# Kernel tuning notes

Hardware: AMD Instinct MI355X
Metric: run time of the kernel (lower is better)

The kernel has to match this reference:

```python
import jax, jax.numpy as jnp
import numpy as np

IN_DIM = 512
OUT_DIM = 256


def setup_inputs() -> dict:
    key = jax.random.key(0)
    ks = jax.random.split(key, 5)
    b, n, d, o = 32, 64, IN_DIM, OUT_DIM
    lim1 = 1.0 / np.sqrt(2 * d)
    lim2 = 1.0 / np.sqrt(o)
    return {
        "x": jax.random.normal(ks[0], (b, n, d), dtype=jnp.float32),
        "W1": jax.random.uniform(ks[1], (o, 2 * d), jnp.float32, -lim1, lim1),
        "b1": jax.random.uniform(ks[2], (o,), jnp.float32, -lim1, lim1),
        "W2": jax.random.uniform(ks[3], (o, o), jnp.float32, -lim2, lim2),
        "b2": jax.random.uniform(ks[4], (o,), jnp.float32, -lim2, lim2),
    }


def reference(x, W1, b1, W2, b2):
    # x: [b, n, d]; fc1 over cat(xi, xj) == xi @ Wa.T + xj @ Wb.T + b1
    b, n, d = x.shape
    Wa, Wb = W1[:, :d], W1[:, d:]
    hi = jnp.einsum("bnd,od->bno", x, Wa)  # [b, n, o]
    hj = jnp.einsum("bnd,od->bno", x, Wb)  # [b, n, o]
    h = hi[:, :, None, :] + hj[:, None, :, :] + b1  # [b, n, n, o]
    y = jax.nn.relu(jnp.einsum("bijo,po->bijp", h, W2) + b2)  # [b, n, n, o]
    mask = ~jnp.eye(n, dtype=bool)  # zero self-pairs
    y = y * mask[None, :, :, None]
    return y.sum(axis=2)  # [b, n, o]
```

## Files before the change

### kernel.cpp

```cpp
#include <hip/hip_runtime.h>
#include <hip/hip_bf16.h>


typedef unsigned short u16;
typedef __attribute__((ext_vector_type(8))) short short8v;
typedef __attribute__((ext_vector_type(4))) short short4v;
typedef __attribute__((ext_vector_type(4))) float float4v;
typedef __attribute__((ext_vector_type(2))) float float2v;

typedef __attribute__((address_space(1))) const unsigned char* gas_ptr;
typedef __attribute__((address_space(3))) unsigned char* las_ptr;

#define FLAG_CONST 0x5EEDF00Du

__device__ __forceinline__ void lds_load16(const void* g, void* l) {
    __builtin_amdgcn_global_load_lds((gas_ptr)g, (las_ptr)l, 16, 0, 0);
}

__device__ __forceinline__ u16 f2bf(float f) {
    unsigned u = __float_as_uint(f);
    return (u16)((u + 0x7fffu + ((u >> 16) & 1u)) >> 16);
}

__device__ __forceinline__ short8v cvt8v(float4v a, float4v b) {
    union { u16 us[8]; short8v v; } o;
    o.us[0] = f2bf(a.x); o.us[1] = f2bf(a.y); o.us[2] = f2bf(a.z); o.us[3] = f2bf(a.w);
    o.us[4] = f2bf(b.x); o.us[5] = f2bf(b.y); o.us[6] = f2bf(b.z); o.us[7] = f2bf(b.w);
    return o.v;
}

#define LDS_TOTAL (66560 + 67584)

__global__ __launch_bounds__(512, 1) void mono_kernel(
    const float* __restrict__ x, const float* __restrict__ W1,
    const float* __restrict__ b1, const float* __restrict__ W2,
    const float* __restrict__ b2,
    u16* __restrict__ Wfb, float* __restrict__ cvec,
    unsigned* __restrict__ flags, float* __restrict__ out) {
    __shared__ __align__(16) unsigned char smem[LDS_TOTAL];
    u16* Xs = (u16*)smem;
    u16* As = (u16*)(smem + 66560);
    u16* Bt = (u16*)(smem + 66560 + 33792);
    u16* Ws = (u16*)(smem + 66560);

    const int bid = blockIdx.x;
    const int tid = threadIdx.x;
    const int lane = tid & 63, w = tid >> 6;
    const int b = ((bid & 7) << 2) | ((bid >> 3) & 3);
    const int pc = bid >> 5;
    const int p0 = pc * 32;
    const int rQ = lane >> 4, rM = lane & 15;

#pragma unroll
    for (int rr = 0; rr < 8; ++rr) {
        int row = w * 8 + rr;
        const float* s = x + (b * 64 + row) * 512 + lane * 8;
        float4v a0 = *(const float4v*)s, a1 = *(const float4v*)(s + 4);
        *(short8v*)&Xs[row * 520 + lane * 8] = cvt8v(a0, a1);
    }

    if (bid < 64) {
        const int q0 = (bid >> 3) * 64;
        const int d0 = (bid & 7) * 64;
        const int pw = q0 & 255;
        const int off = (q0 & 256) * 2;

#pragma unroll
        for (int rr = 0; rr < 4; ++rr) {
            int row = w * 8 + rr * 2 + (lane >> 5);
            int c = lane & 31;
            const float* s = W2 + (pw + row) * 256 + c * 8;
            float4v a0 = *(const float4v*)s, a1 = *(const float4v*)(s + 4);
            *(short8v*)&As[row * 264 + c * 8] = cvt8v(a0, a1);
        }
#pragma unroll
        for (int kk = 0; kk < 2; ++kk) {
            const int m = tid & 15, og = tid >> 4;
            const int o0 = kk * 128 + og * 4;
            const int d4 = m * 4;
            float4v f0 = *(const float4v*)(W1 + (o0 + 0) * 1024 + off + d0 + d4);
            float4v f1 = *(const float4v*)(W1 + (o0 + 1) * 1024 + off + d0 + d4);
            float4v f2 = *(const float4v*)(W1 + (o0 + 2) * 1024 + off + d0 + d4);
            float4v f3 = *(const float4v*)(W1 + (o0 + 3) * 1024 + off + d0 + d4);
            const int u = o0 >> 3, sub = o0 & 7;
#pragma unroll
            for (int dd = 0; dd < 4; ++dd) {
                int d = d4 + dd;
                int usw = u ^ ((d >> 3) & 7);
                union { u16 us[4]; short4v v; } pk;
                pk.us[0] = f2bf(f0[dd]); pk.us[1] = f2bf(f1[dd]);
                pk.us[2] = f2bf(f2[dd]); pk.us[3] = f2bf(f3[dd]);
                *(short4v*)&Bt[d * 264 + usw * 8 + sub] = pk.v;
            }
        }
        __syncthreads();

        const int wm = w >> 1, wn = w & 1;
        float4v pacc[2] = {};
#pragma unroll
        for (int ks = 0; ks < 8; ++ks) {
            short8v a = *(const short8v*)&As[(wm * 16 + rM) * 264 + (ks * 4 + rQ) * 8];
#pragma unroll
            for (int nf = 0; nf < 2; ++nf) {
                int drow = wn * 32 + nf * 16 + rM;
                int ku = (ks * 4 + rQ) ^ ((drow >> 3) & 7);
                short8v bf = *(const short8v*)&Bt[drow * 264 + ku * 8];
                pacc[nf] = __builtin_amdgcn_mfma_f32_16x16x32_bf16(a, bf, pacc[nf], 0, 0, 0);
            }
        }
#pragma unroll
        for (int nf = 0; nf < 2; ++nf)
#pragma unroll
            for (int r = 0; r < 4; ++r) {
                int q = q0 + wm * 16 + rQ * 4 + r;
                int d = d0 + wn * 32 + nf * 16 + rM;
                Wfb[q * 512 + d] = f2bf(pacc[nf][r]);
            }
    } else if (bid == 64 && tid < 256) {
        float acc = b2[tid];
        const float4v* wrow = (const float4v*)(W2 + tid * 256);
#pragma unroll 8
        for (int o4 = 0; o4 < 64; ++o4) {
            float4v wv = wrow[o4];
            float4v bv = *(const float4v*)(b1 + o4 * 4);
            acc += wv.x * bv.x + wv.y * bv.y + wv.z * bv.z + wv.w * bv.w;
        }
        cvec[tid] = acc;
    }

    __syncthreads();
    if (bid <= 64 && tid == 0)
        __hip_atomic_store(&flags[bid * 32], FLAG_CONST, __ATOMIC_RELEASE,
                           __HIP_MEMORY_SCOPE_AGENT);
    if (tid < 65)
        while (__hip_atomic_load(&flags[tid * 32], __ATOMIC_ACQUIRE,
                                 __HIP_MEMORY_SCOPE_AGENT) != FLAG_CONST)
            __builtin_amdgcn_s_sleep(16);
    __syncthreads();

#pragma unroll
    for (int rr = 0; rr < 8; ++rr) {
        int row = w * 8 + rr;
        int q = (row < 32) ? (p0 + row) : (256 + p0 + (row - 32));
        lds_load16(Wfb + q * 512 + lane * 8, (void*)&Ws[row * 520]);
    }
    __syncthreads();

    const int uv = w & 1, rh = w >> 1;
    float4v acc[2] = {};
#pragma unroll
    for (int ks = 0; ks < 16; ++ks) {
        short8v a = *(const short8v*)&Xs[(rh * 16 + rM) * 520 + (ks * 4 + rQ) * 8];
#pragma unroll
        for (int nf = 0; nf < 2; ++nf) {
            int brow = uv * 32 + nf * 16 + rM;
            short8v bf = *(const short8v*)&Ws[brow * 520 + (ks * 4 + rQ) * 8];
            acc[nf] = __builtin_amdgcn_mfma_f32_16x16x32_bf16(a, bf, acc[nf], 0, 0, 0);
        }
    }
    __syncthreads();

    float* Us = (float*)smem;
    float* Vs = Us + 64 * 34;
    float* dst = uv ? Vs : Us;
#pragma unroll
    for (int nf = 0; nf < 2; ++nf)
#pragma unroll
        for (int r = 0; r < 4; ++r)
            dst[(rh * 16 + rQ * 4 + r) * 34 + nf * 16 + rM] = acc[nf][r];
    __syncthreads();

    const int p2 = tid & 15;
    const int ig = tid >> 4;
    float2v cv = *(const float2v*)(cvec + p0 + p2 * 2);
    float2v u2[2], acc2[2];
#pragma unroll
    for (int ii = 0; ii < 2; ++ii) {
        float2v uu = *(const float2v*)&Us[(ig * 2 + ii) * 34 + p2 * 2];
        u2[ii].x = uu.x + cv.x; u2[ii].y = uu.y + cv.y;
        acc2[ii].x = 0.f; acc2[ii].y = 0.f;
    }
#pragma unroll 8
    for (int j = 0; j < 64; ++j) {
        float2v v = *(const float2v*)&Vs[j * 34 + p2 * 2];
#pragma unroll
        for (int ii = 0; ii < 2; ++ii) {
            acc2[ii].x += fmaxf(u2[ii].x + v.x, 0.f);
            acc2[ii].y += fmaxf(u2[ii].y + v.y, 0.f);
        }
    }
#pragma unroll
    for (int ii = 0; ii < 2; ++ii) {
        int i = ig * 2 + ii;
        float2v vd = *(const float2v*)&Vs[i * 34 + p2 * 2];
        acc2[ii].x -= fmaxf(u2[ii].x + vd.x, 0.f);
        acc2[ii].y -= fmaxf(u2[ii].y + vd.y, 0.f);
        *(float2v*)&out[(b * 64 + i) * 256 + p0 + p2 * 2] = acc2[ii];
    }
}

extern "C" void kernel_launch(void* const* d_in, const int* in_sizes, int n_in,
                              void* d_out, int out_size, void* d_ws, size_t ws_size,
                              hipStream_t stream) {
    const float* x  = (const float*)d_in[0];
    const float* W1 = (const float*)d_in[1];
    const float* b1 = (const float*)d_in[2];
    const float* W2 = (const float*)d_in[3];
    const float* b2 = (const float*)d_in[4];
    float* out = (float*)d_out;

    u16* Wfb = (u16*)d_ws;
    float* cvec = (float*)(Wfb + 512 * 512);
    unsigned* flags = (unsigned*)(cvec + 256);

    mono_kernel<<<256, 512, 0, stream>>>(x, W1, b1, W2, b2, Wfb, cvec, flags, out);
}
```

Measured before the change: 24.80 us.

## Remove cross-block flag barrier by recomputing fused weights per block with pipelined staging

Each block now computes its own slice of the fused W2·W1 weights and bias vector in LDS. It streams W1 through double-buffered LDS chunks and interleaves the x-projection MFMAs with the next chunk's weight fusion. This removes the global workspace round trip and the grid-wide spin-wait on atomic flags that serialized all blocks behind the first 65. In exchange every block redoes the weight-fusion GEMM for its 32 output columns, which adds redundant W1 reads and MFMA work across the 256 blocks.

```diff
diff --git a/kernel.cpp b/kernel.cpp
--- a/kernel.cpp
+++ b/kernel.cpp
@@ -8,15 +8,6 @@
 typedef __attribute__((ext_vector_type(4))) float float4v;
 typedef __attribute__((ext_vector_type(2))) float float2v;
 
-typedef __attribute__((address_space(1))) const unsigned char* gas_ptr;
-typedef __attribute__((address_space(3))) unsigned char* las_ptr;
-
-#define FLAG_CONST 0x5EEDF00Du
-
-__device__ __forceinline__ void lds_load16(const void* g, void* l) {
-    __builtin_amdgcn_global_load_lds((gas_ptr)g, (las_ptr)l, 16, 0, 0);
-}
-
 __device__ __forceinline__ u16 f2bf(float f) {
     unsigned u = __float_as_uint(f);
     return (u16)((u + 0x7fffu + ((u >> 16) & 1u)) >> 16);
@@ -29,27 +20,34 @@
     return o.v;
 }
 
-#define LDS_TOTAL (66560 + 67584)
-
-__global__ __launch_bounds__(512, 1) void mono_kernel(
+#define XS_OFF   0
+#define W1_OFF   66560
+#define W1_BUF   33792
+#define W2_OFF   134144
+#define WFS_OFF  151040
+#define WFS_BUF  4608
+#define CVC_OFF  160256
+#define LDS_TOTAL 160512
+
+__global__ __launch_bounds__(512, 1) void solo_kernel(
     const float* __restrict__ x, const float* __restrict__ W1,
     const float* __restrict__ b1, const float* __restrict__ W2,
-    const float* __restrict__ b2,
-    u16* __restrict__ Wfb, float* __restrict__ cvec,
-    unsigned* __restrict__ flags, float* __restrict__ out) {
+    const float* __restrict__ b2, float* __restrict__ out) {
     __shared__ __align__(16) unsigned char smem[LDS_TOTAL];
-    u16* Xs = (u16*)smem;
-    u16* As = (u16*)(smem + 66560);
-    u16* Bt = (u16*)(smem + 66560 + 33792);
-    u16* Ws = (u16*)(smem + 66560);
-
-    const int bid = blockIdx.x;
-    const int tid = threadIdx.x;
+    u16* Xs    = (u16*)(smem + XS_OFF);
+    u16* W1ts0 = (u16*)(smem + W1_OFF);
+    u16* W1ts1 = (u16*)(smem + W1_OFF + W1_BUF);
+    u16* W2s   = (u16*)(smem + W2_OFF);
+    unsigned char* Wfs0 = smem + WFS_OFF;
+    unsigned char* Wfs1 = smem + WFS_OFF + WFS_BUF;
+    float* cvc = (float*)(smem + CVC_OFF);
+
+    const int bid = blockIdx.x, tid = threadIdx.x;
     const int lane = tid & 63, w = tid >> 6;
     const int b = ((bid & 7) << 2) | ((bid >> 3) & 3);
-    const int pc = bid >> 5;
-    const int p0 = pc * 32;
+    const int pc = bid >> 5, p0 = pc * 32;
     const int rQ = lane >> 4, rM = lane & 15;
+    const int dt = w >> 1, pt = w & 1;
 
 #pragma unroll
     for (int rr = 0; rr < 8; ++rr) {
@@ -58,121 +56,133 @@
         float4v a0 = *(const float4v*)s, a1 = *(const float4v*)(s + 4);
         *(short8v*)&Xs[row * 520 + lane * 8] = cvt8v(a0, a1);
     }
-
-    if (bid < 64) {
-        const int q0 = (bid >> 3) * 64;
-        const int d0 = (bid & 7) * 64;
-        const int pw = q0 & 255;
-        const int off = (q0 & 256) * 2;
-
-#pragma unroll
-        for (int rr = 0; rr < 4; ++rr) {
-            int row = w * 8 + rr * 2 + (lane >> 5);
-            int c = lane & 31;
-            const float* s = W2 + (pw + row) * 256 + c * 8;
-            float4v a0 = *(const float4v*)s, a1 = *(const float4v*)(s + 4);
-            *(short8v*)&As[row * 264 + c * 8] = cvt8v(a0, a1);
-        }
+#pragma unroll
+    for (int rr = 0; rr < 2; ++rr) {
+        int row = w * 4 + rr * 2 + (lane >> 5);
+        int c = lane & 31;
+        const float* s = W2 + (p0 + row) * 256 + c * 8;
+        float4v a0 = *(const float4v*)s, a1 = *(const float4v*)(s + 4);
+        *(short8v*)&W2s[row * 264 + c * 8] = cvt8v(a0, a1);
+    }
+    if (w == 0 && lane < 32) {
+        float acc = b2[p0 + lane];
+        const float4v* wr = (const float4v*)(W2 + (p0 + lane) * 256);
+#pragma unroll 8
+        for (int o4 = 0; o4 < 64; ++o4) {
+            float4v wv = wr[o4];
+            float4v bv = *(const float4v*)(b1 + o4 * 4);
+            acc += wv.x * bv.x + wv.y * bv.y + wv.z * bv.z + wv.w * bv.w;
+        }
+        cvc[lane] = acc;
+    }
+
+    const int d4s = (tid & 15) * 4;
+    const int ogs = tid >> 4;
+    float4v sf[2][4];
+    auto stage_load = [&](int ch) {
 #pragma unroll
         for (int kk = 0; kk < 2; ++kk) {
-            const int m = tid & 15, og = tid >> 4;
-            const int o0 = kk * 128 + og * 4;
-            const int d4 = m * 4;
-            float4v f0 = *(const float4v*)(W1 + (o0 + 0) * 1024 + off + d0 + d4);
-            float4v f1 = *(const float4v*)(W1 + (o0 + 1) * 1024 + off + d0 + d4);
-            float4v f2 = *(const float4v*)(W1 + (o0 + 2) * 1024 + off + d0 + d4);
-            float4v f3 = *(const float4v*)(W1 + (o0 + 3) * 1024 + off + d0 + d4);
+            const int o0 = kk * 128 + ogs * 4;
+            const float* s0 = W1 + o0 * 1024 + ((ch >> 3) * 512 + (ch & 7) * 64) + d4s;
+#pragma unroll
+            for (int j = 0; j < 4; ++j)
+                sf[kk][j] = *(const float4v*)(s0 + j * 1024);
+        }
+    };
+    auto stage_write = [&](u16* dst) {
+#pragma unroll
+        for (int kk = 0; kk < 2; ++kk) {
+            const int o0 = kk * 128 + ogs * 4;
             const int u = o0 >> 3, sub = o0 & 7;
 #pragma unroll
             for (int dd = 0; dd < 4; ++dd) {
-                int d = d4 + dd;
+                int d = d4s + dd;
                 int usw = u ^ ((d >> 3) & 7);
                 union { u16 us[4]; short4v v; } pk;
-                pk.us[0] = f2bf(f0[dd]); pk.us[1] = f2bf(f1[dd]);
-                pk.us[2] = f2bf(f2[dd]); pk.us[3] = f2bf(f3[dd]);
-                *(short4v*)&Bt[d * 264 + usw * 8 + sub] = pk.v;
+                pk.us[0] = f2bf(sf[0][dd].x);
+                pk.us[0] = f2bf(sf[kk][0][dd]);
+                pk.us[1] = f2bf(sf[kk][1][dd]);
+                pk.us[2] = f2bf(sf[kk][2][dd]);
+                pk.us[3] = f2bf(sf[kk][3][dd]);
+                *(short4v*)&dst[d * 264 + usw * 8 + sub] = pk.v;
             }
         }
+    };
+
+    stage_load(0);
+    stage_write(W1ts0);
+    __syncthreads();
+
+    float4v Uacc = {0.f, 0.f, 0.f, 0.f}, Vacc = {0.f, 0.f, 0.f, 0.f};
+    const int arow = dt * 16 + rM;
+    const int axor = (arow >> 3) & 7;
+    const int brow = pt * 16 + rM;
+
+    for (int cc = 0; cc < 16; ++cc) {
+        u16* cur = (cc & 1) ? W1ts1 : W1ts0;
+        u16* nxt = (cc & 1) ? W1ts0 : W1ts1;
+        unsigned char* wfcur  = (cc & 1) ? Wfs1 : Wfs0;
+        unsigned char* wfprev = (cc & 1) ? Wfs0 : Wfs1;
+
+        if (cc < 15) stage_load(cc + 1);
+
+        float4v wf = {0.f, 0.f, 0.f, 0.f};
+#pragma unroll
+        for (int ks = 0; ks < 8; ++ks) {
+            short8v a  = *(const short8v*)&cur[arow * 264 + ((ks * 4 + rQ) ^ axor) * 8];
+            short8v bq = *(const short8v*)&W2s[brow * 264 + (ks * 4 + rQ) * 8];
+            wf = __builtin_amdgcn_mfma_f32_16x16x32_bf16(a, bq, wf, 0, 0, 0);
+        }
+        {
+            union { u16 us[4]; short4v v; } pk;
+            pk.us[0] = f2bf(wf[0]); pk.us[1] = f2bf(wf[1]);
+            pk.us[2] = f2bf(wf[2]); pk.us[3] = f2bf(wf[3]);
+            *(short4v*)(wfcur + brow * 144 + (dt * 16 + rQ * 4) * 2) = pk.v;
+        }
+
+        if (cc > 0) {
+            const int k = cc - 1, c = k & 7;
+            if (k < 8) {
+#pragma unroll
+                for (int ks2 = 0; ks2 < 2; ++ks2) {
+                    short8v a  = *(const short8v*)&Xs[arow * 520 + (c * 8 + ks2 * 4 + rQ) * 8];
+                    short8v bq = *(const short8v*)(wfprev + brow * 144 + (ks2 * 4 + rQ) * 16);
+                    Uacc = __builtin_amdgcn_mfma_f32_16x16x32_bf16(a, bq, Uacc, 0, 0, 0);
+                }
+            } else {
+#pragma unroll
+                for (int ks2 = 0; ks2 < 2; ++ks2) {
+                    short8v a  = *(const short8v*)&Xs[arow * 520 + (c * 8 + ks2 * 4 + rQ) * 8];
+                    short8v bq = *(const short8v*)(wfprev + brow * 144 + (ks2 * 4 + rQ) * 16);
+                    Vacc = __builtin_amdgcn_mfma_f32_16x16x32_bf16(a, bq, Vacc, 0, 0, 0);
+                }
+            }
+        }
+
+        if (cc < 15) stage_write(nxt);
         __syncthreads();
-
-        const int wm = w >> 1, wn = w & 1;
-        float4v pacc[2] = {};
-#pragma unroll
-        for (int ks = 0; ks < 8; ++ks) {
-            short8v a = *(const short8v*)&As[(wm * 16 + rM) * 264 + (ks * 4 + rQ) * 8];
-#pragma unroll
-            for (int nf = 0; nf < 2; ++nf) {
-                int drow = wn * 32 + nf * 16 + rM;
-                int ku = (ks * 4 + rQ) ^ ((drow >> 3) & 7);
-                short8v bf = *(const short8v*)&Bt[drow * 264 + ku * 8];
-                pacc[nf] = __builtin_amdgcn_mfma_f32_16x16x32_bf16(a, bf, pacc[nf], 0, 0, 0);
-            }
-        }
-#pragma unroll
-        for (int nf = 0; nf < 2; ++nf)
-#pragma unroll
-            for (int r = 0; r < 4; ++r) {
-                int q = q0 + wm * 16 + rQ * 4 + r;
-                int d = d0 + wn * 32 + nf * 16 + rM;
-                Wfb[q * 512 + d] = f2bf(pacc[nf][r]);
-            }
-    } else if (bid == 64 && tid < 256) {
-        float acc = b2[tid];
-        const float4v* wrow = (const float4v*)(W2 + tid * 256);
-#pragma unroll 8
-        for (int o4 = 0; o4 < 64; ++o4) {
-            float4v wv = wrow[o4];
-            float4v bv = *(const float4v*)(b1 + o4 * 4);
-            acc += wv.x * bv.x + wv.y * bv.y + wv.z * bv.z + wv.w * bv.w;
-        }
-        cvec[tid] = acc;
-    }
-
-    __syncthreads();
-    if (bid <= 64 && tid == 0)
-        __hip_atomic_store(&flags[bid * 32], FLAG_CONST, __ATOMIC_RELEASE,
-                           __HIP_MEMORY_SCOPE_AGENT);
-    if (tid < 65)
-        while (__hip_atomic_load(&flags[tid * 32], __ATOMIC_ACQUIRE,
-                                 __HIP_MEMORY_SCOPE_AGENT) != FLAG_CONST)
-            __builtin_amdgcn_s_sleep(16);
-    __syncthreads();
-
-#pragma unroll
-    for (int rr = 0; rr < 8; ++rr) {
-        int row = w * 8 + rr;
-        int q = (row < 32) ? (p0 + row) : (256 + p0 + (row - 32));
-        lds_load16(Wfb + q * 512 + lane * 8, (void*)&Ws[row * 520]);
-    }
-    __syncthreads();
-
-    const int uv = w & 1, rh = w >> 1;
-    float4v acc[2] = {};
-#pragma unroll
-    for (int ks = 0; ks < 16; ++ks) {
-        short8v a = *(const short8v*)&Xs[(rh * 16 + rM) * 520 + (ks * 4 + rQ) * 8];
-#pragma unroll
-        for (int nf = 0; nf < 2; ++nf) {
-            int brow = uv * 32 + nf * 16 + rM;
-            short8v bf = *(const short8v*)&Ws[brow * 520 + (ks * 4 + rQ) * 8];
-            acc[nf] = __builtin_amdgcn_mfma_f32_16x16x32_bf16(a, bf, acc[nf], 0, 0, 0);
-        }
+    }
+
+#pragma unroll
+    for (int ks2 = 0; ks2 < 2; ++ks2) {
+        short8v a  = *(const short8v*)&Xs[arow * 520 + (7 * 8 + ks2 * 4 + rQ) * 8];
+        short8v bq = *(const short8v*)(Wfs1 + brow * 144 + (ks2 * 4 + rQ) * 16);
+        Vacc = __builtin_amdgcn_mfma_f32_16x16x32_bf16(a, bq, Vacc, 0, 0, 0);
     }
     __syncthreads();
 
     float* Us = (float*)smem;
     float* Vs = Us + 64 * 34;
-    float* dst = uv ? Vs : Us;
-#pragma unroll
-    for (int nf = 0; nf < 2; ++nf)
-#pragma unroll
-        for (int r = 0; r < 4; ++r)
-            dst[(rh * 16 + rQ * 4 + r) * 34 + nf * 16 + rM] = acc[nf][r];
+#pragma unroll
+    for (int r = 0; r < 4; ++r) {
+        Us[(dt * 16 + rQ * 4 + r) * 34 + pt * 16 + rM] = Uacc[r];
+        Vs[(dt * 16 + rQ * 4 + r) * 34 + pt * 16 + rM] = Vacc[r];
+    }
     __syncthreads();
 
     const int p2 = tid & 15;
     const int ig = tid >> 4;
-    float2v cv = *(const float2v*)(cvec + p0 + p2 * 2);
+    float2v cv = *(const float2v*)&cvc[p2 * 2];
     float2v u2[2], acc2[2];
 #pragma unroll
     for (int ii = 0; ii < 2; ++ii) {
@@ -209,9 +219,5 @@
     const float* b2 = (const float*)d_in[4];
     float* out = (float*)d_out;
 
-    u16* Wfb = (u16*)d_ws;
-    float* cvec = (float*)(Wfb + 512 * 512);
-    unsigned* flags = (unsigned*)(cvec + 256);
-
-    mono_kernel<<<256, 512, 0, stream>>>(x, W1, b1, W2, b2, Wfb, cvec, flags, out);
-}
+    solo_kernel<<<256, 512, 0, stream>>>(x, W1, b1, W2, b2, out);
+}
```

After: 30.70 us. 1.24x slower.

## Spread weight-fold precompute across all blocks with targeted flag waits

Applied to the files above, without the earlier changes.

The fused W2·W1 precompute is split into 256 small 32x32 tiles so every block computes one tile, instead of 64 blocks doing 64x64 tiles while the rest wait. Each block now computes its own slice of the bias vector W2·b1+b2 into LDS, which removes a global dependency. Each block waits only on the 32 flags for the tiles it needs rather than all 65. U/V scratch gets its own LDS region, which drops one barrier. In exchange every block does redundant W2 and W1 loads, and the Bt transpose is written with scalar, unswizzled stores that may cause bank conflicts.

```diff
diff --git a/kernel.cpp b/kernel.cpp
--- a/kernel.cpp
+++ b/kernel.cpp
@@ -4,7 +4,6 @@
 
 typedef unsigned short u16;
 typedef __attribute__((ext_vector_type(8))) short short8v;
-typedef __attribute__((ext_vector_type(4))) short short4v;
 typedef __attribute__((ext_vector_type(4))) float float4v;
 typedef __attribute__((ext_vector_type(2))) float float2v;
 
@@ -29,26 +28,37 @@
     return o.v;
 }
 
-#define LDS_TOTAL (66560 + 67584)
-
-__global__ __launch_bounds__(512, 1) void mono_kernel(
+#define XS_OFF   0
+#define WS_OFF   66560
+#define AS_OFF   66560
+#define BT_OFF   83456
+#define UV_OFF   133120
+#define CVC_OFF  150528
+#define LDS_TOTAL 150656
+#define UVS 34
+
+__global__ __launch_bounds__(512, 1) void mono2_kernel(
     const float* __restrict__ x, const float* __restrict__ W1,
     const float* __restrict__ b1, const float* __restrict__ W2,
     const float* __restrict__ b2,
-    u16* __restrict__ Wfb, float* __restrict__ cvec,
-    unsigned* __restrict__ flags, float* __restrict__ out) {
+    u16* __restrict__ Wfb, unsigned* __restrict__ flags,
+    float* __restrict__ out) {
     __shared__ __align__(16) unsigned char smem[LDS_TOTAL];
-    u16* Xs = (u16*)smem;
-    u16* As = (u16*)(smem + 66560);
-    u16* Bt = (u16*)(smem + 66560 + 33792);
-    u16* Ws = (u16*)(smem + 66560);
-
-    const int bid = blockIdx.x;
-    const int tid = threadIdx.x;
+    u16* Xs = (u16*)(smem + XS_OFF);
+    u16* Ws = (u16*)(smem + WS_OFF);
+    u16* As = (u16*)(smem + AS_OFF);
+    u16* Bt = (u16*)(smem + BT_OFF);
+    float* Us = (float*)(smem + UV_OFF);
+    float* Vs = Us + 64 * UVS;
+    float* cvc = (float*)(smem + CVC_OFF);
+
+    const int bid = blockIdx.x, tid = threadIdx.x;
     const int lane = tid & 63, w = tid >> 6;
-    const int b = ((bid & 7) << 2) | ((bid >> 3) & 3);
-    const int pc = bid >> 5;
-    const int p0 = pc * 32;
+    const int b = bid & 31, pc = bid >> 5, p0 = pc * 32;
+    const int qt = bid & 15, dt = bid >> 4;
+    const int q0t = qt * 32, d0 = dt * 32;
+    const int pw = q0t & 255;
+    const int off = (q0t & 256) * 2;
     const int rQ = lane >> 4, rM = lane & 15;
 
 #pragma unroll
@@ -59,83 +69,66 @@
         *(short8v*)&Xs[row * 520 + lane * 8] = cvt8v(a0, a1);
     }
 
-    if (bid < 64) {
-        const int q0 = (bid >> 3) * 64;
-        const int d0 = (bid & 7) * 64;
-        const int pw = q0 & 255;
-        const int off = (q0 & 256) * 2;
-
-#pragma unroll
-        for (int rr = 0; rr < 4; ++rr) {
-            int row = w * 8 + rr * 2 + (lane >> 5);
-            int c = lane & 31;
-            const float* s = W2 + (pw + row) * 256 + c * 8;
-            float4v a0 = *(const float4v*)s, a1 = *(const float4v*)(s + 4);
-            *(short8v*)&As[row * 264 + c * 8] = cvt8v(a0, a1);
-        }
-#pragma unroll
-        for (int kk = 0; kk < 2; ++kk) {
-            const int m = tid & 15, og = tid >> 4;
-            const int o0 = kk * 128 + og * 4;
-            const int d4 = m * 4;
-            float4v f0 = *(const float4v*)(W1 + (o0 + 0) * 1024 + off + d0 + d4);
-            float4v f1 = *(const float4v*)(W1 + (o0 + 1) * 1024 + off + d0 + d4);
-            float4v f2 = *(const float4v*)(W1 + (o0 + 2) * 1024 + off + d0 + d4);
-            float4v f3 = *(const float4v*)(W1 + (o0 + 3) * 1024 + off + d0 + d4);
-            const int u = o0 >> 3, sub = o0 & 7;
-#pragma unroll
-            for (int dd = 0; dd < 4; ++dd) {
-                int d = d4 + dd;
-                int usw = u ^ ((d >> 3) & 7);
-                union { u16 us[4]; short4v v; } pk;
-                pk.us[0] = f2bf(f0[dd]); pk.us[1] = f2bf(f1[dd]);
-                pk.us[2] = f2bf(f2[dd]); pk.us[3] = f2bf(f3[dd]);
-                *(short4v*)&Bt[d * 264 + usw * 8 + sub] = pk.v;
-            }
-        }
-        __syncthreads();
-
-        const int wm = w >> 1, wn = w & 1;
-        float4v pacc[2] = {};
+#pragma unroll
+    for (int rr = 0; rr < 2; ++rr) {
+        int row = w * 4 + rr * 2 + (lane >> 5);
+        int c = lane & 31;
+        const float* s = W2 + (pw + row) * 256 + c * 8;
+        float4v a0 = *(const float4v*)s, a1 = *(const float4v*)(s + 4);
+        *(short8v*)&As[row * 264 + c * 8] = cvt8v(a0, a1);
+    }
+    {
+        const int o = tid & 255;
+        const int dbase = (tid >> 8) * 16;
+        const float* s0 = W1 + o * 1024 + off + d0 + dbase;
+        float4v f[4];
+#pragma unroll
+        for (int q4 = 0; q4 < 4; ++q4) f[q4] = *(const float4v*)(s0 + q4 * 4);
+#pragma unroll
+        for (int dd = 0; dd < 16; ++dd)
+            Bt[(dbase + dd) * 264 + o] = f2bf(f[dd >> 2][dd & 3]);
+    }
+    __syncthreads();
+
+    if (w < 4) {
+        const int wq = w & 1, wd = w >> 1;
+        float4v pacc = {};
 #pragma unroll
         for (int ks = 0; ks < 8; ++ks) {
-            short8v a = *(const short8v*)&As[(wm * 16 + rM) * 264 + (ks * 4 + rQ) * 8];
-#pragma unroll
-            for (int nf = 0; nf < 2; ++nf) {
-                int drow = wn * 32 + nf * 16 + rM;
-                int ku = (ks * 4 + rQ) ^ ((drow >> 3) & 7);
-                short8v bf = *(const short8v*)&Bt[drow * 264 + ku * 8];
-                pacc[nf] = __builtin_amdgcn_mfma_f32_16x16x32_bf16(a, bf, pacc[nf], 0, 0, 0);
-            }
-        }
-#pragma unroll
-        for (int nf = 0; nf < 2; ++nf)
-#pragma unroll
-            for (int r = 0; r < 4; ++r) {
-                int q = q0 + wm * 16 + rQ * 4 + r;
-                int d = d0 + wn * 32 + nf * 16 + rM;
-                Wfb[q * 512 + d] = f2bf(pacc[nf][r]);
-            }
-    } else if (bid == 64 && tid < 256) {
-        float acc = b2[tid];
-        const float4v* wrow = (const float4v*)(W2 + tid * 256);
+            short8v a  = *(const short8v*)&As[(wq * 16 + rM) * 264 + (ks * 4 + rQ) * 8];
+            short8v bf = *(const short8v*)&Bt[(wd * 16 + rM) * 264 + (ks * 4 + rQ) * 8];
+            pacc = __builtin_amdgcn_mfma_f32_16x16x32_bf16(a, bf, pacc, 0, 0, 0);
+        }
+#pragma unroll
+        for (int r = 0; r < 4; ++r) {
+            int q = q0t + wq * 16 + rQ * 4 + r;
+            int d = d0 + wd * 16 + rM;
+            Wfb[q * 512 + d] = f2bf(pacc[r]);
+        }
+    } else if (w == 4 && lane < 32) {
+        float acc = b2[p0 + lane];
+        const float4v* wr = (const float4v*)(W2 + (p0 + lane) * 256);
 #pragma unroll 8
         for (int o4 = 0; o4 < 64; ++o4) {
-            float4v wv = wrow[o4];
+            float4v wv = wr[o4];
             float4v bv = *(const float4v*)(b1 + o4 * 4);
             acc += wv.x * bv.x + wv.y * bv.y + wv.z * bv.z + wv.w * bv.w;
         }
-        cvec[tid] = acc;
-    }
-
-    __syncthreads();
-    if (bid <= 64 && tid == 0)
+        cvc[lane] = acc;
+    }
+    __syncthreads();
+
+    if (tid == 0)
         __hip_atomic_store(&flags[bid * 32], FLAG_CONST, __ATOMIC_RELEASE,
                            __HIP_MEMORY_SCOPE_AGENT);
-    if (tid < 65)
-        while (__hip_atomic_load(&flags[tid * 32], __ATOMIC_ACQUIRE,
+    if (tid < 32) {
+        int qtn = (tid < 16) ? pc : (8 + pc);
+        int dtn = tid & 15;
+        unsigned idx = (unsigned)(dtn * 16 + qtn) * 32;
+        while (__hip_atomic_load(&flags[idx], __ATOMIC_ACQUIRE,
                                  __HIP_MEMORY_SCOPE_AGENT) != FLAG_CONST)
-            __builtin_amdgcn_s_sleep(16);
+            __builtin_amdgcn_s_sleep(8);
+    }
     __syncthreads();
 
 #pragma unroll
@@ -158,31 +151,28 @@
             acc[nf] = __builtin_amdgcn_mfma_f32_16x16x32_bf16(a, bf, acc[nf], 0, 0, 0);
         }
     }
-    __syncthreads();
-
-    float* Us = (float*)smem;
-    float* Vs = Us + 64 * 34;
+
     float* dst = uv ? Vs : Us;
 #pragma unroll
     for (int nf = 0; nf < 2; ++nf)
 #pragma unroll
         for (int r = 0; r < 4; ++r)
-            dst[(rh * 16 + rQ * 4 + r) * 34 + nf * 16 + rM] = acc[nf][r];
+            dst[(rh * 16 + rQ * 4 + r) * UVS + nf * 16 + rM] = acc[nf][r];
     __syncthreads();
 
     const int p2 = tid & 15;
     const int ig = tid >> 4;
-    float2v cv = *(const float2v*)(cvec + p0 + p2 * 2);
+    float2v cv = *(const float2v*)&cvc[p2 * 2];
     float2v u2[2], acc2[2];
 #pragma unroll
     for (int ii = 0; ii < 2; ++ii) {
-        float2v uu = *(const float2v*)&Us[(ig * 2 + ii) * 34 + p2 * 2];
+        float2v uu = *(const float2v*)&Us[(ig * 2 + ii) * UVS + p2 * 2];
         u2[ii].x = uu.x + cv.x; u2[ii].y = uu.y + cv.y;
         acc2[ii].x = 0.f; acc2[ii].y = 0.f;
     }
 #pragma unroll 8
     for (int j = 0; j < 64; ++j) {
-        float2v v = *(const float2v*)&Vs[j * 34 + p2 * 2];
+        float2v v = *(const float2v*)&Vs[j * UVS + p2 * 2];
 #pragma unroll
         for (int ii = 0; ii < 2; ++ii) {
             acc2[ii].x += fmaxf(u2[ii].x + v.x, 0.f);
@@ -192,7 +182,7 @@
 #pragma unroll
     for (int ii = 0; ii < 2; ++ii) {
         int i = ig * 2 + ii;
-        float2v vd = *(const float2v*)&Vs[i * 34 + p2 * 2];
+        float2v vd = *(const float2v*)&Vs[i * UVS + p2 * 2];
         acc2[ii].x -= fmaxf(u2[ii].x + vd.x, 0.f);
         acc2[ii].y -= fmaxf(u2[ii].y + vd.y, 0.f);
         *(float2v*)&out[(b * 64 + i) * 256 + p0 + p2 * 2] = acc2[ii];
@@ -210,8 +200,7 @@
     float* out = (float*)d_out;
 
     u16* Wfb = (u16*)d_ws;
-    float* cvec = (float*)(Wfb + 512 * 512);
-    unsigned* flags = (unsigned*)(cvec + 256);
-
-    mono_kernel<<<256, 512, 0, stream>>>(x, W1, b1, W2, b2, Wfb, cvec, flags, out);
-}
+    unsigned* flags = (unsigned*)(Wfb + 512 * 512);
+
+    mono2_kernel<<<256, 512, 0, stream>>>(x, W1, b1, W2, b2, Wfb, flags, out);
+}
```

Result: faster. 20.88 us (median of 2 runs) (-15.8%).
